# Kernel optimization log

Hardware: AMD Instinct MI355X
Metric: run time of the kernel (lower is better)

## Reference

```python
import jax, jax.numpy as jnp
import numpy as np

NT, NRV, NR = 100000, 200000, 300000  # tile / road_vertex / road node counts
E = 400000                             # edges per edge type
B, H, P, A = 64, 128, 64, 512          # graphs, hidden, player_state_dim, action_dim


def _gat(h_src, h_dst, src, dst, W, a_s, a_d, b, n_dst):
    # PyG GATConv, heads=1, shared lin for src/dst, no self loops (bipartite)
    hs = h_src @ W                      # [Ns, H]
    hd = h_dst @ W                      # [Nd, H]
    e = jax.nn.leaky_relu((hs @ a_s)[src] + (hd @ a_d)[dst], 0.2)  # [E]
    m = jax.ops.segment_max(e, dst, num_segments=n_dst)
    w = jnp.exp(e - m[dst])
    denom = jax.ops.segment_sum(w, dst, num_segments=n_dst)
    alpha = w / jnp.maximum(denom[dst], 1e-16)                      # segment softmax
    out = jax.ops.segment_sum(alpha[:, None] * hs[src], dst, num_segments=n_dst)
    return out + b


def _mean_pool(x, batch, nb):
    s = jax.ops.segment_sum(x, batch, num_segments=nb)
    c = jax.ops.segment_sum(jnp.ones((x.shape[0],), x.dtype), batch, num_segments=nb)
    return s / jnp.maximum(c, 1.0)[:, None]


def setup_inputs():
    ks = iter(jax.random.split(jax.random.key(0), 64))
    f32 = jnp.float32

    def lin(i, o):
        return (jax.random.normal(next(ks), (i, o), f32) / np.float32(np.sqrt(i)))

    d = {}
    d['x_tile'] = jax.random.normal(next(ks), (NT, 8), f32)
    d['x_rv'] = jax.random.normal(next(ks), (NRV, 13), f32)
    d['x_road'] = jax.random.normal(next(ks), (NR, 4), f32)
    d['x_player'] = jax.random.normal(next(ks), (B, P), f32)
    # node encoders
    d['enc_t_W'] = lin(8, H);  d['enc_t_b'] = jnp.zeros((H,), f32)
    d['enc_rv_W'] = lin(13, H); d['enc_rv_b'] = jnp.zeros((H,), f32)
    d['enc_r_W'] = lin(4, H);  d['enc_r_b'] = jnp.zeros((H,), f32)
    # six GAT convs
    for name in ['rv2t', 't2rv', 'r2rv', 'rv2r', 't2r', 'r2t']:
        d[name + '_W'] = lin(H, H)
        d[name + '_as'] = jax.random.normal(next(ks), (H,), f32) * 0.1
        d[name + '_ad'] = jax.random.normal(next(ks), (H,), f32) * 0.1
        d[name + '_b'] = jnp.zeros((H,), f32)
    # player MLP + output head (input: 3H pooled + H player)
    d['fc1_W'] = lin(P, H); d['fc1_b'] = jnp.zeros((H,), f32)
    d['fc2_W'] = lin(H, H); d['fc2_b'] = jnp.zeros((H,), f32)
    d['out_W'] = lin(4 * H, A); d['out_b'] = jnp.zeros((A,), f32)
    # edges (src bounded by source-type count, dst by dest-type count)
    ri = lambda n, hi: jax.random.randint(n, (E,), 0, hi, jnp.int32)
    d['e_rv2t_src'] = ri(next(ks), NRV); d['e_rv2t_dst'] = ri(next(ks), NT)
    d['e_t2rv_src'] = ri(next(ks), NT);  d['e_t2rv_dst'] = ri(next(ks), NRV)
    d['e_r2rv_src'] = ri(next(ks), NR);  d['e_r2rv_dst'] = ri(next(ks), NRV)
    d['e_rv2r_src'] = ri(next(ks), NRV); d['e_rv2r_dst'] = ri(next(ks), NR)
    d['e_t2r_src'] = ri(next(ks), NT);   d['e_t2r_dst'] = ri(next(ks), NR)
    d['e_r2t_src'] = ri(next(ks), NR);   d['e_r2t_dst'] = ri(next(ks), NT)
    # batch assignment per node type
    d['batch_tile'] = jnp.sort(jax.random.randint(next(ks), (NT,), 0, B, jnp.int32))
    d['batch_rv'] = jnp.sort(jax.random.randint(next(ks), (NRV,), 0, B, jnp.int32))
    d['batch_road'] = jnp.sort(jax.random.randint(next(ks), (NR,), 0, B, jnp.int32))
    return d


def reference(x_tile, x_rv, x_road, x_player,
              enc_t_W, enc_t_b, enc_rv_W, enc_rv_b, enc_r_W, enc_r_b,
              rv2t_W, rv2t_as, rv2t_ad, rv2t_b,
              t2rv_W, t2rv_as, t2rv_ad, t2rv_b,
              r2rv_W, r2rv_as, r2rv_ad, r2rv_b,
              rv2r_W, rv2r_as, rv2r_ad, rv2r_b,
              t2r_W, t2r_as, t2r_ad, t2r_b,
              r2t_W, r2t_as, r2t_ad, r2t_b,
              fc1_W, fc1_b, fc2_W, fc2_b, out_W, out_b,
              e_rv2t_src, e_rv2t_dst, e_t2rv_src, e_t2rv_dst,
              e_r2rv_src, e_r2rv_dst, e_rv2r_src, e_rv2r_dst,
              e_t2r_src, e_t2r_dst, e_r2t_src, e_r2t_dst,
              batch_tile, batch_rv, batch_road):
    # node encoders
    h_t = x_tile @ enc_t_W + enc_t_b
    h_rv = x_rv @ enc_rv_W + enc_rv_b
    h_r = x_road @ enc_r_W + enc_r_b
    # hetero GAT, aggr='sum' over edge types per destination node type
    o_t = (_gat(h_rv, h_t, e_rv2t_src, e_rv2t_dst, rv2t_W, rv2t_as, rv2t_ad, rv2t_b, NT)
           + _gat(h_r, h_t, e_r2t_src, e_r2t_dst, r2t_W, r2t_as, r2t_ad, r2t_b, NT))
    o_rv = (_gat(h_t, h_rv, e_t2rv_src, e_t2rv_dst, t2rv_W, t2rv_as, t2rv_ad, t2rv_b, NRV)
            + _gat(h_r, h_rv, e_r2rv_src, e_r2rv_dst, r2rv_W, r2rv_as, r2rv_ad, r2rv_b, NRV))
    o_r = (_gat(h_rv, h_r, e_rv2r_src, e_rv2r_dst, rv2r_W, rv2r_as, rv2r_ad, rv2r_b, NR)
           + _gat(h_t, h_r, e_t2r_src, e_t2r_dst, t2r_W, t2r_as, t2r_ad, t2r_b, NR))
    # global mean pool per node type, concat -> [B, 3H]
    x_all = jnp.concatenate([_mean_pool(o_t, batch_tile, B),
                             _mean_pool(o_rv, batch_rv, B),
                             _mean_pool(o_r, batch_road, B)], axis=1)
    # player branch
    p = jax.nn.relu(x_player @ fc1_W + fc1_b)
    p = jax.nn.relu(p @ fc2_W + fc2_b)
    x = jnp.concatenate([x_all, p], axis=1)  # [B, 4H]
    return x @ out_W + out_b                 # [B, A]
```

## Files before the change

kernel.cpp:

```cpp
#include <hip/hip_runtime.h>


constexpr int kNT = 100000, kNRV = 200000, kNR = 300000, kE = 400000;
constexpr int kTOTE = 6 * kE;
constexpr int kSLOT = 1088;
constexpr int kPSZ  = 6 * kSLOT;
constexpr int kNB   = 367;

constexpr long long OFF_C    = 0;
constexpr long long OFF_VS   = 13056;
constexpr long long OFF_VD   = 13176;
constexpr long long OFF_P    = 13296;
constexpr long long OFF_XCAT = 19824;
constexpr long long OFF_LS   = 52592;
constexpr long long OFF_LD   = 1252592;
constexpr long long OFF_PB   = 52592;
constexpr long long OFF_W16  = 2452592;
constexpr long long OFF_DR2  = 3652592;
constexpr long long OFF_XR   = 6052592;

__constant__ const int kLSB[6] = {0, 200000, 300000, 600000, 800000, 900000};
__constant__ const int kDRB[6] = {0, 100000, 300000, 500000, 800000, 1100000};
__constant__ const int kDLEN[6] = {100000, 200000, 200000, 300000, 300000, 100000};

__global__ __launch_bounds__(256) void precompute_kernel(
    const float* encW_t, const float* encb_t,
    const float* encW_rv, const float* encb_rv,
    const float* encW_r, const float* encb_r,
    const float* W0, const float* as0, const float* ad0,
    const float* W1, const float* as1, const float* ad1,
    const float* W2, const float* as2, const float* ad2,
    const float* W3, const float* as3, const float* ad3,
    const float* W4, const float* as4, const float* ad4,
    const float* W5, const float* as5, const float* ad5,
    float* Cws, float* vsw, float* vdw)
{
  const float* encW[3] = {encW_t, encW_rv, encW_r};
  const float* encb[3] = {encb_t, encb_rv, encb_r};
  const int    Ks[3]   = {8, 13, 4};
  const float* Wv[6]  = {W0, W1, W2, W3, W4, W5};
  const float* asv[6] = {as0, as1, as2, as3, as4, as5};
  const float* adv[6] = {ad0, ad1, ad2, ad3, ad4, ad5};
  const int srcT[6] = {1, 0, 2, 1, 0, 2};
  const int dstT[6] = {0, 1, 1, 2, 2, 0};

  __shared__ float Cl[2176];
  __shared__ float wv[128];

  int et = blockIdx.x;
  int tid = threadIdx.x;
  int st = srcT[et], dt = dstT[et];
  const float* eW = encW[st];
  const float* eB = encb[st];
  int K = Ks[st];
  const float* W = Wv[et];
  const float* a_s = asv[et];
  const float* a_d = adv[et];
  float* Cslot = Cws + et * 2176;

  for (int idx = tid; idx < (K + 1) * 128; idx += 256) {
    int r = idx >> 7, j = idx & 127;
    const float* row = (r < K) ? (eW + r * 128) : eB;
    float acc = 0.f;
    for (int m = 0; m < 128; ++m) acc += row[m] * W[m * 128 + j];
    int o = (r < K) ? (r * 128 + j) : (2048 + j);
    Cl[o] = acc;
    Cslot[o] = acc;
  }
  if (tid < 128) {
    float acc = 0.f;
    for (int j = 0; j < 128; ++j) acc += W[tid * 128 + j] * a_d[j];
    wv[tid] = acc;
  }
  __syncthreads();
  if (tid <= K) {
    const float* row = (tid < K) ? (Cl + tid * 128) : (Cl + 2048);
    float acc = 0.f;
    for (int j = 0; j < 128; ++j) acc += row[j] * a_s[j];
    vsw[et * 20 + (tid < K ? tid : 16)] = acc;
  }
  int KD = Ks[dt];
  if (tid >= 32 && tid <= 32 + KD) {
    int k = tid - 32;
    const float* row = (k < KD) ? (encW[dt] + k * 128) : encb[dt];
    float acc = 0.f;
    for (int m = 0; m < 128; ++m) acc += row[m] * wv[m];
    vdw[et * 20 + (k < KD ? k : 16)] = acc;
  }
}

template <int K, int RH>
__device__ __forceinline__ void prep_one(
    const float* __restrict__ xr, float bf,
    const float* __restrict__ vsA, const float* __restrict__ vsB,
    const float* __restrict__ vdA, const float* __restrict__ vdB,
    float* lsA, float* lsB, float* ldA, float* ldB,
    float2* dr2A, float2* dr2B, _Float16* xrec)
{
  float a0 = 0.f, a1 = 0.f, a2 = 0.f, a3 = 0.f;
#pragma unroll
  for (int k = 0; k < K; ++k) {
    float xv = xr[k];
    a0 += xv * vsA[k]; a1 += xv * vsB[k];
    a2 += xv * vdA[k]; a3 += xv * vdB[k];
    xrec[k] = (_Float16)xv;
  }
#pragma unroll
  for (int k = K; k < RH; ++k) xrec[k] = (_Float16)0.f;
  *lsA = a0 + vsA[16];
  *lsB = a1 + vsB[16];
  *ldA = a2 + vdA[16];
  *ldB = a3 + vdB[16];
  *dr2A = make_float2(0.f, bf);
  *dr2B = make_float2(0.f, bf);
}

__global__ __launch_bounds__(256) void prep_kernel(
    const float* __restrict__ x_t, const float* __restrict__ x_rv,
    const float* __restrict__ x_r,
    const int* __restrict__ bt, const int* __restrict__ brv,
    const int* __restrict__ br,
    const float* __restrict__ vsw, const float* __restrict__ vdw,
    float* __restrict__ LS, float* __restrict__ LD,
    float2* __restrict__ DR2, _Float16* __restrict__ XR)
{
  int n = blockIdx.x * 256 + threadIdx.x;
  if (n >= kNT + kNRV + kNR) return;
  if (n < kNT) {
    prep_one<8, 8>(x_t + n * 8, (float)bt[n],
                   vsw + 1 * 20, vsw + 4 * 20, vdw + 0 * 20, vdw + 5 * 20,
                   LS + 200000 + n, LS + 800000 + n,
                   LD + 0 + n, LD + 1100000 + n,
                   DR2 + 0 + n, DR2 + 1100000 + n,
                   XR + (long long)n * 8);
  } else if (n < kNT + kNRV) {
    int m = n - kNT;
    prep_one<13, 16>(x_rv + m * 13, (float)brv[m],
                     vsw + 0 * 20, vsw + 3 * 20, vdw + 1 * 20, vdw + 2 * 20,
                     LS + 0 + m, LS + 600000 + m,
                     LD + 100000 + m, LD + 300000 + m,
                     DR2 + 100000 + m, DR2 + 300000 + m,
                     XR + 800000 + (long long)m * 16);
  } else {
    int m = n - kNT - kNRV;
    prep_one<4, 4>(x_r + m * 4, (float)br[m],
                   vsw + 2 * 20, vsw + 5 * 20, vdw + 3 * 20, vdw + 4 * 20,
                   LS + 300000 + m, LS + 900000 + m,
                   LD + 500000 + m, LD + 800000 + m,
                   DR2 + 500000 + m, DR2 + 800000 + m,
                   XR + 4000000 + (long long)m * 4);
  }
}

__global__ __launch_bounds__(256) void passA_kernel(
    const int* s0, const int* s1, const int* s2,
    const int* s3, const int* s4, const int* s5,
    const int* d0, const int* d1, const int* d2,
    const int* d3, const int* d4, const int* d5,
    const float* __restrict__ LS, const float* __restrict__ LD,
    float* __restrict__ DR2f, _Float16* __restrict__ W16)
{
  int i = blockIdx.x * 256 + threadIdx.x;
  if (i >= kTOTE) return;
  int et = i / kE;
  int e = i - et * kE;
  const int* sp; const int* dp;
  switch (et) {
    case 0: sp = s0; dp = d0; break;
    case 1: sp = s1; dp = d1; break;
    case 2: sp = s2; dp = d2; break;
    case 3: sp = s3; dp = d3; break;
    case 4: sp = s4; dp = d4; break;
    default: sp = s5; dp = d5; break;
  }
  int lsb = kLSB[et], drb = kDRB[et];
  int s = sp[e], d = dp[e];
  float t = LS[lsb + s] + LD[drb + d];
  t = t > 0.f ? t : 0.2f * t;
  _Float16 h = (_Float16)__expf(t);
  W16[i] = h;
  unsafeAtomicAdd(&DR2f[(long long)(drb + d) * 2], (float)h);
}

template <int K, int RH>
__device__ __forceinline__ void passB_loop(
    const int* __restrict__ sp, const int* __restrict__ dp,
    int drb, int dlen, long long xrb,
    const _Float16* __restrict__ W16et, const float2* __restrict__ DR2,
    const _Float16* __restrict__ XR, float* __restrict__ lp,
    int start, int stride)
{
  int nItems = kE + dlen;
  for (int i = start; i < nItems; i += stride) {
    if (i < kE) {
      int s = sp[i], d = dp[i];
      float2 rec = DR2[drb + d];
      float w = (float)W16et[i];
      float alpha = w / fmaxf(rec.x, 1e-16f);
      int b = (int)rec.y;
      const _Float16* xp = XR + xrb + (long long)s * RH;
      float xv[K];
      if constexpr (RH == 4) {
        union { uint2 u; _Float16 h[4]; } U;
        U.u = *(const uint2*)xp;
#pragma unroll
        for (int k = 0; k < K; ++k) xv[k] = (float)U.h[k];
      } else if constexpr (RH == 8) {
        union { uint4 u; _Float16 h[8]; } U;
        U.u = *(const uint4*)xp;
#pragma unroll
        for (int k = 0; k < K; ++k) xv[k] = (float)U.h[k];
      } else {
        union { uint4 u[2]; _Float16 h[16]; } U;
        U.u[0] = *(const uint4*)xp;
        U.u[1] = *(const uint4*)(xp + 8);
#pragma unroll
        for (int k = 0; k < K; ++k) xv[k] = (float)U.h[k];
      }
#pragma unroll
      for (int k = 0; k < K; ++k) atomicAdd(lp + k * 64 + b, alpha * xv[k]);
    } else {
      int j = i - kE;
      float2 rec = DR2[drb + j];
      if (rec.x > 0.f) atomicAdd(lp + 1024 + (int)rec.y, 1.f);
    }
  }
}

__global__ __launch_bounds__(256) void passB_kernel(
    const int* s0, const int* s1, const int* s2,
    const int* s3, const int* s4, const int* s5,
    const int* d0, const int* d1, const int* d2,
    const int* d3, const int* d4, const int* d5,
    const _Float16* __restrict__ W16, const float2* __restrict__ DR2,
    const _Float16* __restrict__ XR, float* __restrict__ PB)
{
  __shared__ float lp[kSLOT];
  for (int j = threadIdx.x; j < kSLOT; j += 256) lp[j] = 0.f;
  __syncthreads();
  int et  = blockIdx.x / kNB;
  int blk = blockIdx.x - et * kNB;
  int start = blk * 256 + threadIdx.x;
  int stride = kNB * 256;
  int drb = kDRB[et], dlen = kDLEN[et];
  const _Float16* W16et = W16 + (long long)et * kE;
  switch (et) {
    case 0: passB_loop<13,16>(s0, d0, drb, dlen, 800000,  W16et, DR2, XR, lp, start, stride); break;
    case 1: passB_loop< 8, 8>(s1, d1, drb, dlen, 0,       W16et, DR2, XR, lp, start, stride); break;
    case 2: passB_loop< 4, 4>(s2, d2, drb, dlen, 4000000, W16et, DR2, XR, lp, start, stride); break;
    case 3: passB_loop<13,16>(s3, d3, drb, dlen, 800000,  W16et, DR2, XR, lp, start, stride); break;
    case 4: passB_loop< 8, 8>(s4, d4, drb, dlen, 0,       W16et, DR2, XR, lp, start, stride); break;
    default: passB_loop<4, 4>(s5, d5, drb, dlen, 4000000, W16et, DR2, XR, lp, start, stride); break;
  }
  __syncthreads();
  float* dst = PB + (long long)blockIdx.x * kSLOT;
  for (int j = threadIdx.x; j < kSLOT; j += 256) dst[j] = lp[j];
}

__global__ __launch_bounds__(256) void reduceP_kernel(
    const float* __restrict__ PB, float* __restrict__ P)
{
  int j = blockIdx.x * 256 + threadIdx.x;
  if (j >= kPSZ) return;
  int et = j / kSLOT;
  int jj = j - et * kSLOT;
  const float* base = PB + (long long)et * kNB * kSLOT + jj;
  float s = 0.f;
  int b = 0;
  for (; b + 8 <= kNB; b += 8) {
    float v0 = base[(long long)(b + 0) * kSLOT];
    float v1 = base[(long long)(b + 1) * kSLOT];
    float v2 = base[(long long)(b + 2) * kSLOT];
    float v3 = base[(long long)(b + 3) * kSLOT];
    float v4 = base[(long long)(b + 4) * kSLOT];
    float v5 = base[(long long)(b + 5) * kSLOT];
    float v6 = base[(long long)(b + 6) * kSLOT];
    float v7 = base[(long long)(b + 7) * kSLOT];
    s += ((v0 + v1) + (v2 + v3)) + ((v4 + v5) + (v6 + v7));
  }
  for (; b < kNB; ++b) s += base[(long long)b * kSLOT];
  P[j] = s;
}

__device__ __forceinline__ int lowb(const int* a, int n, int v) {
  int lo = 0, hi = n;
  while (lo < hi) { int mid = (lo + hi) >> 1; if (a[mid] < v) lo = mid + 1; else hi = mid; }
  return lo;
}

__global__ __launch_bounds__(128) void finalize_kernel(
    const int* __restrict__ bt, const int* __restrict__ brv, const int* __restrict__ br,
    const float* __restrict__ xp,
    const float* __restrict__ fc1W, const float* __restrict__ fc1b,
    const float* __restrict__ fc2W, const float* __restrict__ fc2b,
    const float* __restrict__ b_rv2t, const float* __restrict__ b_r2t,
    const float* __restrict__ b_t2rv, const float* __restrict__ b_r2rv,
    const float* __restrict__ b_rv2r, const float* __restrict__ b_t2r,
    const float* __restrict__ Cws, const float* __restrict__ P,
    float* __restrict__ xcat)
{
  int b = blockIdx.x, tid = threadIdx.x;
  __shared__ float xps[64];
  __shared__ float p1s[128];
  __shared__ int cnts[3];
  if (tid < 64) xps[tid] = xp[b * 64 + tid];
  if (tid < 3) {
    const int* ba = (tid == 0) ? bt : (tid == 1 ? brv : br);
    int N = (tid == 0) ? kNT : (tid == 1 ? kNRV : kNR);
    cnts[tid] = lowb(ba, N, b + 1) - lowb(ba, N, b);
  }
  __syncthreads();
  float a = fc1b[tid];
  for (int k = 0; k < 64; ++k) a += xps[k] * fc1W[k * 128 + tid];
  p1s[tid] = fmaxf(a, 0.f);
  __syncthreads();
  float a2 = fc2b[tid];
  for (int k = 0; k < 128; ++k) a2 += p1s[k] * fc2W[k * 128 + tid];
  xcat[b * 512 + 384 + tid] = fmaxf(a2, 0.f);
  const int etA[3] = {0, 1, 3}, etB[3] = {5, 2, 4};
  const int KAv[3] = {13, 8, 13}, KBv[3] = {4, 4, 8};
  for (int t3 = 0; t3 < 3; ++t3) {
    int eA = etA[t3], eB = etB[t3];
    const float* CA = Cws + eA * 2176;
    const float* CB = Cws + eB * 2176;
    const float* pA = P + eA * kSLOT;
    const float* pB = P + eB * kSLOT;
    float cA = pA[1024 + b];
    float cB = pB[1024 + b];
    float v = cA * CA[2048 + tid] + cB * CB[2048 + tid];
    for (int k = 0; k < KAv[t3]; ++k) v += pA[k * 64 + b] * CA[k * 128 + tid];
    for (int k = 0; k < KBv[t3]; ++k) v += pB[k * 64 + b] * CB[k * 128 + tid];
    float cnt = (float)max(cnts[t3], 1);
    const float* bb1 = (t3 == 0) ? b_rv2t : (t3 == 1 ? b_t2rv : b_rv2r);
    const float* bb2 = (t3 == 0) ? b_r2t  : (t3 == 1 ? b_r2rv : b_t2r);
    xcat[b * 512 + t3 * 128 + tid] = v / cnt + bb1[tid] + bb2[tid];
  }
}

__global__ __launch_bounds__(256) void out_kernel(
    const float* __restrict__ xcat, const float* __restrict__ outW,
    const float* __restrict__ outb, float* __restrict__ out)
{
  int g = blockIdx.x * 256 + threadIdx.x;
  int r = g >> 9, c = g & 511;
  const float* xr = xcat + r * 512;
  float acc = outb[c];
  for (int k = 0; k < 512; ++k) acc += xr[k] * outW[k * 512 + c];
  out[g] = acc;
}

extern "C" void kernel_launch(void* const* d_in, const int* in_sizes, int n_in,
                              void* d_out, int out_size, void* d_ws, size_t ws_size,
                              hipStream_t stream) {
  const float* x_tile   = (const float*)d_in[0];
  const float* x_rv     = (const float*)d_in[1];
  const float* x_road   = (const float*)d_in[2];
  const float* x_player = (const float*)d_in[3];
  const float* enc_t_W  = (const float*)d_in[4];
  const float* enc_t_b  = (const float*)d_in[5];
  const float* enc_rv_W = (const float*)d_in[6];
  const float* enc_rv_b = (const float*)d_in[7];
  const float* enc_r_W  = (const float*)d_in[8];
  const float* enc_r_b  = (const float*)d_in[9];
  const float* W[6]; const float* As[6]; const float* Ad[6]; const float* Bb[6];
  for (int et = 0; et < 6; ++et) {
    W[et]  = (const float*)d_in[10 + 4 * et];
    As[et] = (const float*)d_in[11 + 4 * et];
    Ad[et] = (const float*)d_in[12 + 4 * et];
    Bb[et] = (const float*)d_in[13 + 4 * et];
  }
  const float* fc1W = (const float*)d_in[34];
  const float* fc1b = (const float*)d_in[35];
  const float* fc2W = (const float*)d_in[36];
  const float* fc2b = (const float*)d_in[37];
  const float* outW = (const float*)d_in[38];
  const float* outb = (const float*)d_in[39];
  const int* esrc[6]; const int* edst[6];
  for (int et = 0; et < 6; ++et) {
    esrc[et] = (const int*)d_in[40 + 2 * et];
    edst[et] = (const int*)d_in[41 + 2 * et];
  }
  const int* batch_t  = (const int*)d_in[52];
  const int* batch_rv = (const int*)d_in[53];
  const int* batch_r  = (const int*)d_in[54];

  float* wsF = (float*)d_ws;
  float* Cws  = wsF + OFF_C;
  float* vsw  = wsF + OFF_VS;
  float* vdw  = wsF + OFF_VD;
  float* P    = wsF + OFF_P;
  float* xcat = wsF + OFF_XCAT;
  float* LS   = wsF + OFF_LS;
  float* LD   = wsF + OFF_LD;
  float* PB   = wsF + OFF_PB;
  _Float16* W16 = (_Float16*)(wsF + OFF_W16);
  float2* DR2 = (float2*)(wsF + OFF_DR2);
  float* DR2f = wsF + OFF_DR2;
  _Float16* XR = (_Float16*)(wsF + OFF_XR);
  float* out  = (float*)d_out;

  precompute_kernel<<<6, 256, 0, stream>>>(
      enc_t_W, enc_t_b, enc_rv_W, enc_rv_b, enc_r_W, enc_r_b,
      W[0], As[0], Ad[0], W[1], As[1], Ad[1], W[2], As[2], Ad[2],
      W[3], As[3], Ad[3], W[4], As[4], Ad[4], W[5], As[5], Ad[5],
      Cws, vsw, vdw);

  prep_kernel<<<(kNT + kNRV + kNR + 255) / 256, 256, 0, stream>>>(
      x_tile, x_rv, x_road, batch_t, batch_rv, batch_r, vsw, vdw,
      LS, LD, DR2, XR);

  passA_kernel<<<(kTOTE + 255) / 256, 256, 0, stream>>>(
      esrc[0], esrc[1], esrc[2], esrc[3], esrc[4], esrc[5],
      edst[0], edst[1], edst[2], edst[3], edst[4], edst[5],
      LS, LD, DR2f, W16);

  passB_kernel<<<6 * kNB, 256, 0, stream>>>(
      esrc[0], esrc[1], esrc[2], esrc[3], esrc[4], esrc[5],
      edst[0], edst[1], edst[2], edst[3], edst[4], edst[5],
      W16, DR2, XR, PB);

  reduceP_kernel<<<(kPSZ + 255) / 256, 256, 0, stream>>>(PB, P);

  finalize_kernel<<<64, 128, 0, stream>>>(
      batch_t, batch_rv, batch_r, x_player,
      fc1W, fc1b, fc2W, fc2b,
      Bb[0], Bb[5], Bb[1], Bb[2], Bb[3], Bb[4],
      Cws, P, xcat);

  out_kernel<<<128, 256, 0, stream>>>(xcat, outW, outb, out);

  (void)in_sizes; (void)n_in; (void)out_size; (void)ws_size;
}
```

Measured before the change: 506.7 us.

## Pack per-node records into fp16, vectorize edge passes, split reductions

```diff
diff --git a/kernel.cpp b/kernel.cpp
--- a/kernel.cpp
+++ b/kernel.cpp
@@ -2,25 +2,30 @@
 
 
 constexpr int kNT = 100000, kNRV = 200000, kNR = 300000, kE = 400000;
+constexpr int kEh   = kE / 2;
 constexpr int kTOTE = 6 * kE;
 constexpr int kSLOT = 1088;
 constexpr int kPSZ  = 6 * kSLOT;
-constexpr int kNB   = 367;
+constexpr int kNB   = 256;
+
+struct alignas(8) DRec { _Float16 ld; unsigned short batch; float denom; };
+
+typedef _Float16 h2v __attribute__((ext_vector_type(2)));
 
 constexpr long long OFF_C    = 0;
 constexpr long long OFF_VS   = 13056;
 constexpr long long OFF_VD   = 13176;
 constexpr long long OFF_P    = 13296;
-constexpr long long OFF_XCAT = 19824;
-constexpr long long OFF_LS   = 52592;
-constexpr long long OFF_LD   = 1252592;
-constexpr long long OFF_PB   = 52592;
-constexpr long long OFF_W16  = 2452592;
-constexpr long long OFF_DR2  = 3652592;
-constexpr long long OFF_XR   = 6052592;
-
-__constant__ const int kLSB[6] = {0, 200000, 300000, 600000, 800000, 900000};
-__constant__ const int kDRB[6] = {0, 100000, 300000, 500000, 800000, 1100000};
+constexpr long long OFF_P8   = 19824;
+constexpr long long OFF_XCAT = 72048;
+constexpr long long OFF_LS16 = 104816;
+constexpr long long OFF_W16  = 704816;
+constexpr long long OFF_DREC = 1904816;
+constexpr long long OFF_XR   = 4304816;
+constexpr long long OFF_PB   = 6904816;
+
+__constant__ const int kLSB[6]  = {0, 200000, 300000, 600000, 800000, 900000};
+__constant__ const int kDRB[6]  = {0, 100000, 300000, 500000, 800000, 1100000};
 __constant__ const int kDLEN[6] = {100000, 200000, 200000, 300000, 300000, 100000};
 
 __global__ __launch_bounds__(256) void precompute_kernel(
@@ -44,58 +49,63 @@
   const int srcT[6] = {1, 0, 2, 1, 0, 2};
   const int dstT[6] = {0, 1, 1, 2, 2, 0};
 
-  __shared__ float Cl[2176];
-  __shared__ float wv[128];
-
-  int et = blockIdx.x;
+  int et = blockIdx.x >> 2;
+  int jc = blockIdx.x & 3;
   int tid = threadIdx.x;
   int st = srcT[et], dt = dstT[et];
   const float* eW = encW[st];
   const float* eB = encb[st];
   int K = Ks[st];
   const float* W = Wv[et];
-  const float* a_s = asv[et];
-  const float* a_d = adv[et];
+
   float* Cslot = Cws + et * 2176;
-
-  for (int idx = tid; idx < (K + 1) * 128; idx += 256) {
-    int r = idx >> 7, j = idx & 127;
+  for (int idx = tid; idx < (K + 1) * 32; idx += 256) {
+    int r = idx >> 5, jj = idx & 31;
+    int j = jc * 32 + jj;
     const float* row = (r < K) ? (eW + r * 128) : eB;
     float acc = 0.f;
     for (int m = 0; m < 128; ++m) acc += row[m] * W[m * 128 + j];
-    int o = (r < K) ? (r * 128 + j) : (2048 + j);
-    Cl[o] = acc;
-    Cslot[o] = acc;
-  }
-  if (tid < 128) {
-    float acc = 0.f;
-    for (int j = 0; j < 128; ++j) acc += W[tid * 128 + j] * a_d[j];
-    wv[tid] = acc;
-  }
-  __syncthreads();
-  if (tid <= K) {
-    const float* row = (tid < K) ? (Cl + tid * 128) : (Cl + 2048);
-    float acc = 0.f;
-    for (int j = 0; j < 128; ++j) acc += row[j] * a_s[j];
-    vsw[et * 20 + (tid < K ? tid : 16)] = acc;
-  }
-  int KD = Ks[dt];
-  if (tid >= 32 && tid <= 32 + KD) {
-    int k = tid - 32;
-    const float* row = (k < KD) ? (encW[dt] + k * 128) : encb[dt];
-    float acc = 0.f;
-    for (int m = 0; m < 128; ++m) acc += row[m] * wv[m];
-    vdw[et * 20 + (k < KD ? k : 16)] = acc;
+    Cslot[(r < K) ? (r * 128 + j) : (2048 + j)] = acc;
+  }
+
+  if (jc == 0) {
+    __shared__ float us[128], wvs[128];
+    const float* a_s = asv[et];
+    const float* a_d = adv[et];
+    if (tid < 128) {
+      float acc = 0.f;
+      for (int j = 0; j < 128; ++j) acc += W[tid * 128 + j] * a_s[j];
+      us[tid] = acc;
+    } else {
+      int m = tid - 128;
+      float acc = 0.f;
+      for (int j = 0; j < 128; ++j) acc += W[m * 128 + j] * a_d[j];
+      wvs[m] = acc;
+    }
+    __syncthreads();
+    if (tid <= K) {
+      const float* row = (tid < K) ? (eW + tid * 128) : eB;
+      float acc = 0.f;
+      for (int m = 0; m < 128; ++m) acc += row[m] * us[m];
+      vsw[et * 20 + (tid < K ? tid : 16)] = acc;
+    }
+    int KD = Ks[dt];
+    if (tid >= 32 && tid <= 32 + KD) {
+      int k = tid - 32;
+      const float* row = (k < KD) ? (encW[dt] + k * 128) : encb[dt];
+      float acc = 0.f;
+      for (int m = 0; m < 128; ++m) acc += row[m] * wvs[m];
+      vdw[et * 20 + (k < KD ? k : 16)] = acc;
+    }
   }
 }
 
 template <int K, int RH>
 __device__ __forceinline__ void prep_one(
-    const float* __restrict__ xr, float bf,
+    const float* __restrict__ xr, unsigned short b,
     const float* __restrict__ vsA, const float* __restrict__ vsB,
     const float* __restrict__ vdA, const float* __restrict__ vdB,
-    float* lsA, float* lsB, float* ldA, float* ldB,
-    float2* dr2A, float2* dr2B, _Float16* xrec)
+    _Float16* lsA, _Float16* lsB, DRec* drA, DRec* drB, _Float16* xrec)
 {
   float a0 = 0.f, a1 = 0.f, a2 = 0.f, a3 = 0.f;
 #pragma unroll
@@ -107,12 +117,12 @@
   }
 #pragma unroll
   for (int k = K; k < RH; ++k) xrec[k] = (_Float16)0.f;
-  *lsA = a0 + vsA[16];
-  *lsB = a1 + vsB[16];
-  *ldA = a2 + vdA[16];
-  *ldB = a3 + vdB[16];
-  *dr2A = make_float2(0.f, bf);
-  *dr2B = make_float2(0.f, bf);
+  *lsA = (_Float16)(a0 + vsA[16]);
+  *lsB = (_Float16)(a1 + vsB[16]);
+  DRec rA; rA.ld = (_Float16)(a2 + vdA[16]); rA.batch = b; rA.denom = 0.f;
+  DRec rB; rB.ld = (_Float16)(a3 + vdB[16]); rB.batch = b; rB.denom = 0.f;
+  *drA = rA;
+  *drB = rB;
 }
 
 __global__ __launch_bounds__(256) void prep_kernel(
@@ -121,33 +131,30 @@
     const int* __restrict__ bt, const int* __restrict__ brv,
     const int* __restrict__ br,
     const float* __restrict__ vsw, const float* __restrict__ vdw,
-    float* __restrict__ LS, float* __restrict__ LD,
-    float2* __restrict__ DR2, _Float16* __restrict__ XR)
+    _Float16* __restrict__ LS16, DRec* __restrict__ DRC,
+    _Float16* __restrict__ XR)
 {
   int n = blockIdx.x * 256 + threadIdx.x;
   if (n >= kNT + kNRV + kNR) return;
   if (n < kNT) {
-    prep_one<8, 8>(x_t + n * 8, (float)bt[n],
+    prep_one<8, 8>(x_t + n * 8, (unsigned short)bt[n],
                    vsw + 1 * 20, vsw + 4 * 20, vdw + 0 * 20, vdw + 5 * 20,
-                   LS + 200000 + n, LS + 800000 + n,
-                   LD + 0 + n, LD + 1100000 + n,
-                   DR2 + 0 + n, DR2 + 1100000 + n,
+                   LS16 + 200000 + n, LS16 + 800000 + n,
+                   DRC + 0 + n, DRC + 1100000 + n,
                    XR + (long long)n * 8);
   } else if (n < kNT + kNRV) {
     int m = n - kNT;
-    prep_one<13, 16>(x_rv + m * 13, (float)brv[m],
+    prep_one<13, 16>(x_rv + m * 13, (unsigned short)brv[m],
                      vsw + 0 * 20, vsw + 3 * 20, vdw + 1 * 20, vdw + 2 * 20,
-                     LS + 0 + m, LS + 600000 + m,
-                     LD + 100000 + m, LD + 300000 + m,
-                     DR2 + 100000 + m, DR2 + 300000 + m,
+                     LS16 + 0 + m, LS16 + 600000 + m,
+                     DRC + 100000 + m, DRC + 300000 + m,
                      XR + 800000 + (long long)m * 16);
   } else {
     int m = n - kNT - kNRV;
-    prep_one<4, 4>(x_r + m * 4, (float)br[m],
+    prep_one<4, 4>(x_r + m * 4, (unsigned short)br[m],
                    vsw + 2 * 20, vsw + 5 * 20, vdw + 3 * 20, vdw + 4 * 20,
-                   LS + 300000 + m, LS + 900000 + m,
-                   LD + 500000 + m, LD + 800000 + m,
-                   DR2 + 500000 + m, DR2 + 800000 + m,
+                   LS16 + 300000 + m, LS16 + 900000 + m,
+                   DRC + 500000 + m, DRC + 800000 + m,
                    XR + 4000000 + (long long)m * 4);
   }
 }
@@ -157,13 +164,13 @@
     const int* s3, const int* s4, const int* s5,
     const int* d0, const int* d1, const int* d2,
     const int* d3, const int* d4, const int* d5,
-    const float* __restrict__ LS, const float* __restrict__ LD,
-    float* __restrict__ DR2f, _Float16* __restrict__ W16)
-{
-  int i = blockIdx.x * 256 + threadIdx.x;
-  if (i >= kTOTE) return;
-  int et = i / kE;
-  int e = i - et * kE;
+    const _Float16* __restrict__ LS16, DRec* __restrict__ DRC,
+    _Float16* __restrict__ W16)
+{
+  int idx = blockIdx.x * 256 + threadIdx.x;
+  if (idx >= kTOTE / 2) return;
+  int et = idx / kEh;
+  int p = idx - et * kEh;
   const int* sp; const int* dp;
   switch (et) {
     case 0: sp = s0; dp = d0; break;
@@ -174,56 +181,74 @@
     default: sp = s5; dp = d5; break;
   }
   int lsb = kLSB[et], drb = kDRB[et];
-  int s = sp[e], d = dp[e];
-  float t = LS[lsb + s] + LD[drb + d];
-  t = t > 0.f ? t : 0.2f * t;
-  _Float16 h = (_Float16)__expf(t);
-  W16[i] = h;
-  unsafeAtomicAdd(&DR2f[(long long)(drb + d) * 2], (float)h);
+  int2 ss = ((const int2*)sp)[p];
+  int2 dd = ((const int2*)dp)[p];
+  DRec* r0 = &DRC[drb + dd.x];
+  DRec* r1 = &DRC[drb + dd.y];
+  float t0 = (float)LS16[lsb + ss.x] + (float)r0->ld;
+  float t1 = (float)LS16[lsb + ss.y] + (float)r1->ld;
+  t0 = t0 > 0.f ? t0 : 0.2f * t0;
+  t1 = t1 > 0.f ? t1 : 0.2f * t1;
+  _Float16 h0 = (_Float16)__expf(t0);
+  _Float16 h1 = (_Float16)__expf(t1);
+  h2v hh; hh.x = h0; hh.y = h1;
+  ((h2v*)W16)[idx] = hh;
+  unsafeAtomicAdd(&r0->denom, (float)h0);
+  unsafeAtomicAdd(&r1->denom, (float)h1);
+}
+
+template <int RH>
+__device__ __forceinline__ void loadX(const _Float16* __restrict__ xp, float* xv) {
+  if constexpr (RH == 4) {
+    union { uint2 u; _Float16 h[4]; } U;
+    U.u = *(const uint2*)xp;
+#pragma unroll
+    for (int k = 0; k < RH; ++k) xv[k] = (float)U.h[k];
+  } else if constexpr (RH == 8) {
+    union { uint4 u; _Float16 h[8]; } U;
+    U.u = *(const uint4*)xp;
+#pragma unroll
+    for (int k = 0; k < RH; ++k) xv[k] = (float)U.h[k];
+  } else {
+    union { uint4 u[2]; _Float16 h[16]; } U;
+    U.u[0] = *(const uint4*)xp;
+    U.u[1] = *(const uint4*)(xp + 8);
+#pragma unroll
+    for (int k = 0; k < RH; ++k) xv[k] = (float)U.h[k];
+  }
 }
 
 template <int K, int RH>
 __device__ __forceinline__ void passB_loop(
     const int* __restrict__ sp, const int* __restrict__ dp,
     int drb, int dlen, long long xrb,
-    const _Float16* __restrict__ W16et, const float2* __restrict__ DR2,
+    const h2v* __restrict__ W2et, const DRec* __restrict__ DRC,
     const _Float16* __restrict__ XR, float* __restrict__ lp,
     int start, int stride)
 {
-  int nItems = kE + dlen;
-  for (int i = start; i < nItems; i += stride) {
-    if (i < kE) {
-      int s = sp[i], d = dp[i];
-      float2 rec = DR2[drb + d];
-      float w = (float)W16et[i];
-      float alpha = w / fmaxf(rec.x, 1e-16f);
-      int b = (int)rec.y;
-      const _Float16* xp = XR + xrb + (long long)s * RH;
-      float xv[K];
-      if constexpr (RH == 4) {
-        union { uint2 u; _Float16 h[4]; } U;
-        U.u = *(const uint2*)xp;
-#pragma unroll
-        for (int k = 0; k < K; ++k) xv[k] = (float)U.h[k];
-      } else if constexpr (RH == 8) {
-        union { uint4 u; _Float16 h[8]; } U;
-        U.u = *(const uint4*)xp;
-#pragma unroll
-        for (int k = 0; k < K; ++k) xv[k] = (float)U.h[k];
-      } else {
-        union { uint4 u[2]; _Float16 h[16]; } U;
-        U.u[0] = *(const uint4*)xp;
-        U.u[1] = *(const uint4*)(xp + 8);
-#pragma unroll
-        for (int k = 0; k < K; ++k) xv[k] = (float)U.h[k];
-      }
-#pragma unroll
-      for (int k = 0; k < K; ++k) atomicAdd(lp + k * 64 + b, alpha * xv[k]);
-    } else {
-      int j = i - kE;
-      float2 rec = DR2[drb + j];
-      if (rec.x > 0.f) atomicAdd(lp + 1024 + (int)rec.y, 1.f);
+  for (int p = start; p < kEh; p += stride) {
+    int2 ss = ((const int2*)sp)[p];
+    int2 dd = ((const int2*)dp)[p];
+    h2v ww = W2et[p];
+    DRec r0 = DRC[drb + dd.x];
+    DRec r1 = DRC[drb + dd.y];
+    const _Float16* xp0 = XR + xrb + (long long)ss.x * RH;
+    const _Float16* xp1 = XR + xrb + (long long)ss.y * RH;
+    float xv0[RH], xv1[RH];
+    loadX<RH>(xp0, xv0);
+    loadX<RH>(xp1, xv1);
+    float a0 = (float)ww.x / fmaxf(r0.denom, 1e-16f);
+    float a1 = (float)ww.y / fmaxf(r1.denom, 1e-16f);
+    int b0 = r0.batch, b1 = r1.batch;
+#pragma unroll
+    for (int k = 0; k < K; ++k) {
+      atomicAdd(lp + k * 64 + b0, a0 * xv0[k]);
+      atomicAdd(lp + k * 64 + b1, a1 * xv1[k]);
     }
+  }
+  for (int j = start; j < dlen; j += stride) {
+    DRec r = DRC[drb + j];
+    if (r.denom > 0.f) atomicAdd(lp + 1024 + r.batch, 1.f);
   }
 }
 
@@ -232,7 +257,7 @@
     const int* s3, const int* s4, const int* s5,
     const int* d0, const int* d1, const int* d2,
     const int* d3, const int* d4, const int* d5,
-    const _Float16* __restrict__ W16, const float2* __restrict__ DR2,
+    const _Float16* __restrict__ W16, const DRec* __restrict__ DRC,
     const _Float16* __restrict__ XR, float* __restrict__ PB)
 {
   __shared__ float lp[kSLOT];
@@ -243,42 +268,44 @@
   int start = blk * 256 + threadIdx.x;
   int stride = kNB * 256;
   int drb = kDRB[et], dlen = kDLEN[et];
-  const _Float16* W16et = W16 + (long long)et * kE;
+  const h2v* W2et = (const h2v*)(W16 + (long long)et * kE);
   switch (et) {
-    case 0: passB_loop<13,16>(s0, d0, drb, dlen, 800000,  W16et, DR2, XR, lp, start, stride); break;
-    case 1: passB_loop< 8, 8>(s1, d1, drb, dlen, 0,       W16et, DR2, XR, lp, start, stride); break;
-    case 2: passB_loop< 4, 4>(s2, d2, drb, dlen, 4000000, W16et, DR2, XR, lp, start, stride); break;
-    case 3: passB_loop<13,16>(s3, d3, drb, dlen, 800000,  W16et, DR2, XR, lp, start, stride); break;
-    case 4: passB_loop< 8, 8>(s4, d4, drb, dlen, 0,       W16et, DR2, XR, lp, start, stride); break;
-    default: passB_loop<4, 4>(s5, d5, drb, dlen, 4000000, W16et, DR2, XR, lp, start, stride); break;
+    case 0: passB_loop<13,16>(s0, d0, drb, dlen, 800000,  W2et, DRC, XR, lp, start, stride); break;
+    case 1: passB_loop< 8, 8>(s1, d1, drb, dlen, 0,       W2et, DRC, XR, lp, start, stride); break;
+    case 2: passB_loop< 4, 4>(s2, d2, drb, dlen, 4000000, W2et, DRC, XR, lp, start, stride); break;
+    case 3: passB_loop<13,16>(s3, d3, drb, dlen, 800000,  W2et, DRC, XR, lp, start, stride); break;
+    case 4: passB_loop< 8, 8>(s4, d4, drb, dlen, 0,       W2et, DRC, XR, lp, start, stride); break;
+    default: passB_loop<4, 4>(s5, d5, drb, dlen, 4000000, W2et, DRC, XR, lp, start, stride); break;
   }
   __syncthreads();
   float* dst = PB + (long long)blockIdx.x * kSLOT;
   for (int j = threadIdx.x; j < kSLOT; j += 256) dst[j] = lp[j];
 }
 
-__global__ __launch_bounds__(256) void reduceP_kernel(
-    const float* __restrict__ PB, float* __restrict__ P)
-{
-  int j = blockIdx.x * 256 + threadIdx.x;
+__global__ __launch_bounds__(256) void reduce1_kernel(
+    const float* __restrict__ PB, float* __restrict__ P8)
+{
+  int jb = blockIdx.x % 26;
+  int c  = blockIdx.x / 26;
+  int j = jb * 256 + threadIdx.x;
   if (j >= kPSZ) return;
   int et = j / kSLOT;
   int jj = j - et * kSLOT;
-  const float* base = PB + (long long)et * kNB * kSLOT + jj;
+  const float* base = PB + ((long long)(et * kNB + c * 32)) * kSLOT + jj;
   float s = 0.f;
-  int b = 0;
-  for (; b + 8 <= kNB; b += 8) {
-    float v0 = base[(long long)(b + 0) * kSLOT];
-    float v1 = base[(long long)(b + 1) * kSLOT];
-    float v2 = base[(long long)(b + 2) * kSLOT];
-    float v3 = base[(long long)(b + 3) * kSLOT];
-    float v4 = base[(long long)(b + 4) * kSLOT];
-    float v5 = base[(long long)(b + 5) * kSLOT];
-    float v6 = base[(long long)(b + 6) * kSLOT];
-    float v7 = base[(long long)(b + 7) * kSLOT];
-    s += ((v0 + v1) + (v2 + v3)) + ((v4 + v5) + (v6 + v7));
-  }
-  for (; b < kNB; ++b) s += base[(long long)b * kSLOT];
+#pragma unroll 8
+  for (int t = 0; t < 32; ++t) s += base[(long long)t * kSLOT];
+  P8[c * kPSZ + j] = s;
+}
+
+__global__ __launch_bounds__(256) void reduce2_kernel(
+    const float* __restrict__ P8, float* __restrict__ P)
+{
+  int j = blockIdx.x * 256 + threadIdx.x;
+  if (j >= kPSZ) return;
+  float s = 0.f;
+#pragma unroll
+  for (int c = 0; c < 8; ++c) s += P8[c * kPSZ + j];
   P[j] = s;
 }
 
@@ -389,17 +416,16 @@
   float* vsw  = wsF + OFF_VS;
   float* vdw  = wsF + OFF_VD;
   float* P    = wsF + OFF_P;
+  float* P8   = wsF + OFF_P8;
   float* xcat = wsF + OFF_XCAT;
-  float* LS   = wsF + OFF_LS;
-  float* LD   = wsF + OFF_LD;
+  _Float16* LS16 = (_Float16*)(wsF + OFF_LS16);
+  _Float16* W16  = (_Float16*)(wsF + OFF_W16);
+  DRec* DRC  = (DRec*)(wsF + OFF_DREC);
+  _Float16* XR = (_Float16*)(wsF + OFF_XR);
   float* PB   = wsF + OFF_PB;
-  _Float16* W16 = (_Float16*)(wsF + OFF_W16);
-  float2* DR2 = (float2*)(wsF + OFF_DR2);
-  float* DR2f = wsF + OFF_DR2;
-  _Float16* XR = (_Float16*)(wsF + OFF_XR);
   float* out  = (float*)d_out;
 
-  precompute_kernel<<<6, 256, 0, stream>>>(
+  precompute_kernel<<<24, 256, 0, stream>>>(
       enc_t_W, enc_t_b, enc_rv_W, enc_rv_b, enc_r_W, enc_r_b,
       W[0], As[0], Ad[0], W[1], As[1], Ad[1], W[2], As[2], Ad[2],
       W[3], As[3], Ad[3], W[4], As[4], Ad[4], W[5], As[5], Ad[5],
@@ -407,19 +433,20 @@
 
   prep_kernel<<<(kNT + kNRV + kNR + 255) / 256, 256, 0, stream>>>(
       x_tile, x_rv, x_road, batch_t, batch_rv, batch_r, vsw, vdw,
-      LS, LD, DR2, XR);
-
-  passA_kernel<<<(kTOTE + 255) / 256, 256, 0, stream>>>(
+      LS16, DRC, XR);
+
+  passA_kernel<<<(kTOTE / 2 + 255) / 256, 256, 0, stream>>>(
       esrc[0], esrc[1], esrc[2], esrc[3], esrc[4], esrc[5],
       edst[0], edst[1], edst[2], edst[3], edst[4], edst[5],
-      LS, LD, DR2f, W16);
+      LS16, DRC, W16);
 
   passB_kernel<<<6 * kNB, 256, 0, stream>>>(
       esrc[0], esrc[1], esrc[2], esrc[3], esrc[4], esrc[5],
       edst[0], edst[1], edst[2], edst[3], edst[4], edst[5],
-      W16, DR2, XR, PB);
-
-  reduceP_kernel<<<(kPSZ + 255) / 256, 256, 0, stream>>>(PB, P);
+      W16, DRC, XR, PB);
+
+  reduce1_kernel<<<26 * 8, 256, 0, stream>>>(PB, P8);
+  reduce2_kernel<<<26, 256, 0, stream>>>(P8, P);
 
   finalize_kernel<<<64, 128, 0, stream>>>(
       batch_t, batch_rv, batch_r, x_player,
```

Result: slower. 571.0 us (+12.7%).
